# Kernel optimization log

Measured on AMD Instinct MI355X. Metric: run time of the kernel, lower is better.

## Reference

```python
import jax, jax.numpy as jnp
import numpy as np

# ---- constants from init_kwargs (mode='local', channel='G') ----
MEAN = 127.5
STD = 50.0
BINS = np.array([-2.4, -1.6, -0.8, 0.0, 0.8, 1.6, 2.4])
NB = len(BINS) + 1            # 8 quantization levels
DIST = [1, 2, 3]
THETA = [0.0, np.pi / 4, np.pi / 2, 3 * np.pi / 4]
MASK = 17
STRIDE = 4
BIN_EDGES = 0.5 + BINS / 6.0
# skimage greycomatrix offsets: (round(sin(t)*d), round(cos(t)*d)), ordered d-major
OFFSETS = [(int(np.round(np.sin(t) * d)), int(np.round(np.cos(t) * d)))
           for d in DIST for t in THETA]


def setup_inputs() -> dict:
    key = jax.random.key(0)
    x = jax.random.uniform(key, (8, 3, 256, 256), dtype=jnp.float32) * 255.0
    return {"x": x}


def _features(x):
    img = x[:, 1, :, :]                       # channel 'G'
    img = jnp.where(img < 10.0, 0.0, img)     # imgs[imgs < 10] = 0
    B, H, W = img.shape
    N = (H - MASK) // STRIDE + 1              # 60 windows per axis

    # sliding windows -> (B, N, N, MASK, MASK)
    r = (jnp.arange(N) * STRIDE)[:, None] + jnp.arange(MASK)[None, :]
    win = img[:, r[:, None, :, None], r[None, :, None, :]]
    Nw = B * N * N
    flat = win.reshape(Nw, MASK * MASK)

    # ---- stat over nonzero pixels (numpy population std) ----
    mask = flat != 0.0
    n_safe = jnp.maximum(mask.sum(-1), 1).astype(flat.dtype)
    mean = jnp.where(mask, flat, 0.0).sum(-1) / n_safe
    std = jnp.sqrt((jnp.where(mask, flat - mean[:, None], 0.0) ** 2).sum(-1) / n_safe)
    mx = jnp.where(mask, flat, -jnp.inf).max(-1)
    mn = jnp.where(mask, flat, jnp.inf).min(-1)
    stat = jnp.stack([mean, std, (mx - mean) / (std + 1e-9), (mean - mn) / (std + 1e-9)], -1)

    # ---- quantize ----
    q = jnp.digitize(((flat - MEAN) / STD + 3.0) / 6.0, jnp.asarray(BIN_EDGES, flat.dtype))

    # ---- histogram (density over ALL pixels, drop first & last bin) ----
    onehot = (q[..., None] == jnp.arange(NB)).astype(flat.dtype)
    hist_feat = onehot.sum(1)[:, 1:NB - 1] / flat.shape[1]   # (Nw, len(BINS)-1)

    # ---- GLCM per (dist, theta) offset, symmetric + normed ----
    qm = q.reshape(Nw, MASK, MASK)
    rows = jnp.arange(Nw)[:, None]
    glcms = []
    for dr, dc in OFFSETS:
        if dc >= 0:
            i = qm[:, :MASK - dr, :MASK - dc]
            j = qm[:, dr:, dc:]
        else:
            i = qm[:, :MASK - dr, -dc:]
            j = qm[:, dr:, :MASK + dc]
        pair = (i * NB + j).reshape(Nw, -1)
        cnt = jnp.zeros((Nw, NB * NB), flat.dtype).at[rows, pair].add(1.0)
        P = cnt.reshape(Nw, NB, NB)
        P = P + P.transpose(0, 2, 1)                               # symmetric
        P = P / jnp.maximum(P.sum((1, 2), keepdims=True), 1e-12)   # normed
        glcms.append(P)
    G = jnp.stack(glcms, 1)          # (Nw, 12, NB, NB)
    g = G[:, :, 1:, 1:]              # crop level 0 (zeros)
    L = NB - 1

    # greycoprops renormalizes the (cropped) GLCM internally
    Pn = g / jnp.maximum(g.sum((2, 3), keepdims=True), 1e-12)
    I = jnp.arange(L, dtype=flat.dtype)
    diff2 = (I[:, None] - I[None, :]) ** 2
    contrast = (Pn * diff2).sum((2, 3))
    homog = (Pn / (1.0 + diff2)).sum((2, 3))
    energy = jnp.sqrt((Pn ** 2).sum((2, 3)))
    Pi = Pn.sum(3)
    Pj = Pn.sum(2)
    mui = (Pi * I).sum(-1)
    muj = (Pj * I).sum(-1)
    sdi = jnp.sqrt((Pi * (I - mui[..., None]) ** 2).sum(-1))
    sdj = jnp.sqrt((Pj * (I - muj[..., None]) ** 2).sum(-1))
    cov = (Pn * (I[:, None] - mui[..., None, None]) * (I[None, :] - muj[..., None, None])).sum((2, 3))
    corr = jnp.where(sdi * sdj < 1e-15, 1.0, cov / jnp.maximum(sdi * sdj, 1e-15))
    entropy = -(g * jnp.log2(g + 1e-8)).sum((2, 3))   # on cropped, non-renormed g

    glcm_feat = jnp.concatenate([contrast, homog, energy, corr, entropy], -1)  # (Nw, 60)
    feats = jnp.concatenate([stat, hist_feat, glcm_feat], -1)                  # (Nw, 70)

    # windows with max == 0 yield all-zero feature vectors
    feats = jnp.where((flat.max(-1) == 0.0)[:, None], 0.0, feats)

    Fdim = feats.shape[-1]
    feats = feats.reshape(B, N, N, Fdim)
    total = feats.sum((1, 2))
    nz = (feats != 0).sum((1, 2)).astype(flat.dtype)
    return total / (nz + 1e-9)            # (B, 70)


def reference(x):
    return _features(x)
```

## Files before the change

### kernel.cpp

```cpp
#include <hip/hip_runtime.h>
#include <cmath>

#define NPIX   289
#define NU     10
#define NF     70
#define NWX    60
#define IMG_W  256
#define IMG_HW 65536
#define NWIN   28800
#define ACC    560
#define WPB    4
#define NBLK   (NWIN / WPB)

__device__ __constant__ int c_s2u[12] = {0,1,2,3,4,1,5,3,6,7,8,9};

constexpr int DRu[NU] = {0, 1, 1, 1, 0, 2, 0, 2, 3, 2};
constexpr int DCu[NU] = {1, 1, 0,-1, 2, 0, 3, 2, 0,-2};
constexpr int JOFF[NU] = {1, 18, 17, 16, 2, 34, 3, 36, 51, 32};
constexpr float INV2N[NU] = {1.f/544.f, 1.f/512.f, 1.f/544.f, 1.f/512.f, 1.f/510.f,
                             1.f/510.f, 1.f/476.f, 1.f/450.f, 1.f/476.f, 1.f/450.f};

struct CMs { unsigned m[10]; };
constexpr CMs mkcm(int dc) {
    CMs c{};
    for (int t = 0; t < NPIX; ++t) {
        int col = t % 17;
        bool ok = (dc > 0) ? (col >= dc) : (col <= 16 + dc);
        if (ok) c.m[t >> 5] |= 1u << (t & 31);
    }
    return c;
}
constexpr CMs CMp1 = mkcm(1), CMp2 = mkcm(2), CMp3 = mkcm(3);
constexpr CMs CMn1 = mkcm(-1), CMn2 = mkcm(-2);

struct alignas(32) FtE { float w, d2, inv, si, sii, sij, q0, q1; };
struct FtTab { FtE e[28]; };
constexpr FtTab mkft() {
    FtTab t{};
    int n = 0;
    for (int a = 1; a <= 7; ++a)
        for (int b = a; b <= 7; ++b) {
            int i = a - 1, j = b - 1;
            float w  = (a == b) ? 1.f : 2.f;
            float d2 = (float)((i - j) * (i - j));
            t.e[n] = FtE{w, d2, 1.f / (1.f + d2),
                         0.5f * (float)(i + j),
                         0.5f * (float)(i * i + j * j),
                         (float)(i * j), 0.f, 0.f};
            ++n;
        }
    return t;
}
__device__ __constant__ FtTab c_ft = mkft();

template<int O>
__device__ __forceinline__ int gcnt(const unsigned* M, const unsigned* ma) {
    constexpr int wq = JOFF[O] >> 5;
    constexpr int rr = JOFF[O] & 31;
    int acc = 0;
#pragma unroll
    for (int w = 0; w < 9; ++w) {
        unsigned sh = (rr == 0) ? M[w + wq]
                    : __builtin_amdgcn_alignbit(M[w + wq + 1], M[w + wq], rr);
        acc += __popc(ma[w] & sh);
    }
    return acc;
}

__device__ __forceinline__ float wsum(float v){ for(int o=32;o;o>>=1) v += __shfl_xor(v,o,64); return v; }
__device__ __forceinline__ float wmax(float v){ for(int o=32;o;o>>=1) v = fmaxf(v,__shfl_xor(v,o,64)); return v; }
__device__ __forceinline__ float wmin(float v){ for(int o=32;o;o>>=1) v = fminf(v,__shfl_xor(v,o,64)); return v; }

__global__ __launch_bounds__(256, 4) void feat_kernel(const float* __restrict__ x,
                                                      float* __restrict__ ptot,
                                                      float* __restrict__ pnz,
                                                      int setmask) {
    __shared__ float s_g[WPB][NU * 28];
    __shared__ float s_uf[WPB][5][NU];
    __shared__ float s_s10[WPB][10];

    const int lane = threadIdx.x & 63;
    const int wid  = threadIdx.x >> 6;
    const int widx = blockIdx.x * WPB + wid;
    const int b    = widx / 3600;
    const int rem  = widx - b * 3600;
    const int wy   = rem / NWX;
    const int wx   = rem - wy * NWX;
    const float* img = x + (size_t)(b * 3 + 1) * IMG_HW + (wy * 4) * IMG_W + wx * 4;

    float* gl  = s_g[wid];
    float (*uf)[NU] = s_uf[wid];
    float* s10 = s_s10[wid];

    const int l49 = (lane < 49) ? lane : 48;
    const int ba  = l49 / 7 + 1;
    const int bb  = l49 - (ba - 1) * 7 + 1;
    const unsigned long long xm0a = (ba & 1) ? 0ull : ~0ull;
    const unsigned long long xm1a = (ba & 2) ? 0ull : ~0ull;
    const unsigned long long xm2a = (ba & 4) ? 0ull : ~0ull;
    const unsigned long long xm0b = (bb & 1) ? 0ull : ~0ull;
    const unsigned long long xm1b = (bb & 2) ? 0ull : ~0ull;
    const unsigned long long xm2b = (bb & 4) ? 0ull : ~0ull;

    float lsum = 0.f, lss = 0.f, lmax = -1e30f, lmin = 1e30f;
    int n = 0, c1 = 0, c2 = 0, c3 = 0, c4 = 0, c5 = 0, c6 = 0;
    unsigned ma32[10], mb32[12];
#pragma unroll
    for (int k = 0; k < 5; ++k) {
        const int t = lane + k * 64;
        float val = 0.f;
        if (t < NPIX) {
            const int r = t / 17;
            float p = img[r * (IMG_W - 17) + t];
            val = (p < 10.f) ? 0.f : p;
        }
        int qq = min((int)fmaf(val, 0.025f, 0.8125f), 7);
        lsum += val;
        float d = (val != 0.f) ? (val - 127.5f) : 0.f;
        lss = fmaf(d, d, lss);
        lmax = fmaxf(lmax, val);
        lmin = fminf(lmin, (val != 0.f) ? val : 1e30f);
        unsigned long long p0 = __ballot(qq & 1);
        unsigned long long p1 = __ballot(qq & 2);
        unsigned long long p2 = __ballot(qq & 4);
        n  += __popcll(p0 | p1 | p2);
        c1 += __popcll(p0 & ~p1 & ~p2);
        c2 += __popcll(~p0 & p1 & ~p2);
        c3 += __popcll(p0 & p1 & ~p2);
        c4 += __popcll(~p0 & ~p1 & p2);
        c5 += __popcll(p0 & ~p1 & p2);
        c6 += __popcll(~p0 & p1 & p2);
        unsigned long long mA = (p0 ^ xm0a) & (p1 ^ xm1a) & (p2 ^ xm2a);
        unsigned long long mB = (p0 ^ xm0b) & (p1 ^ xm1b) & (p2 ^ xm2b);
        ma32[2*k]   = (unsigned)mA;  ma32[2*k+1] = (unsigned)(mA >> 32);
        mb32[2*k]   = (unsigned)mB;  mb32[2*k+1] = (unsigned)(mB >> 32);
    }
    mb32[10] = 0u; mb32[11] = 0u;

    if (n == 0) return;

    const float fn   = (float)n;
    const float sum  = wsum(lsum);
    const float ss   = wsum(lss);
    const float mx   = wmax(lmax);
    const float mn   = wmin(lmin);
    const float mean = sum / fn;
    const float mc   = mean - 127.5f;
    const float var  = fmaxf(ss / fn - mc * mc, 0.f);
    const float stdv = sqrtf(var);

    if (lane == 0) {
        s10[0] = mean;
        s10[1] = stdv;
        s10[2] = (mx - mean) / (stdv + 1e-9f);
        s10[3] = (mean - mn) / (stdv + 1e-9f);
        s10[4] = (float)c1 * (1.f / 289.f);
        s10[5] = (float)c2 * (1.f / 289.f);
        s10[6] = (float)c3 * (1.f / 289.f);
        s10[7] = (float)c4 * (1.f / 289.f);
        s10[8] = (float)c5 * (1.f / 289.f);
        s10[9] = (float)c6 * (1.f / 289.f);
    }

    int cnta[NU];
    {
        unsigned mv[12]; mv[10] = 0u; mv[11] = 0u;
        cnta[2] = gcnt<2>(mb32, ma32);
        cnta[5] = gcnt<5>(mb32, ma32);
        cnta[8] = gcnt<8>(mb32, ma32);
#pragma unroll
        for (int w = 0; w < 10; ++w) mv[w] = mb32[w] & CMp1.m[w];
        cnta[0] = gcnt<0>(mv, ma32);
        cnta[1] = gcnt<1>(mv, ma32);
#pragma unroll
        for (int w = 0; w < 10; ++w) mv[w] = mb32[w] & CMp2.m[w];
        cnta[4] = gcnt<4>(mv, ma32);
        cnta[7] = gcnt<7>(mv, ma32);
#pragma unroll
        for (int w = 0; w < 10; ++w) mv[w] = mb32[w] & CMp3.m[w];
        cnta[6] = gcnt<6>(mv, ma32);
#pragma unroll
        for (int w = 0; w < 10; ++w) mv[w] = mb32[w] & CMn1.m[w];
        cnta[3] = gcnt<3>(mv, ma32);
#pragma unroll
        for (int w = 0; w < 10; ++w) mv[w] = mb32[w] & CMn2.m[w];
        cnta[9] = gcnt<9>(mv, ma32);
    }

    const int partner = (bb - 1) * 7 + (ba - 1);
    const int amin  = min(ba, bb);
    const int idx28 = 8 * (amin - 1) - ((amin * (amin - 1)) >> 1) + (max(ba, bb) - amin);
    const bool wr   = (lane < 49) && (ba <= bb);
#pragma unroll
    for (int o = 0; o < NU; ++o) {
        int pc = __shfl(cnta[o], partner, 64);
        float g = (float)(cnta[o] + pc) * INV2N[o];
        if (wr) gl[o * 28 + idx28] = g;
    }

    const int fo  = lane & 15;
    const int sub = lane >> 4;
    float gsum=0.f, entU=0.f, conU=0.f, homU=0.f, g2=0.f, siU=0.f, siiU=0.f, sijU=0.f;
    if (fo < NU) {
#pragma unroll
        for (int i = 0; i < 7; ++i) {
            const int e = sub + 4 * i;
            FtE c = c_ft.e[e];
            float g  = gl[fo * 28 + e];
            float gw = g * c.w;
            float l  = __log2f(g + 1e-8f);
            gsum += gw;
            entU  = fmaf(gw, l,      entU);
            conU  = fmaf(gw, c.d2,   conU);
            homU  = fmaf(gw, c.inv,  homU);
            g2    = fmaf(gw, g,      g2);
            siU   = fmaf(gw, c.si,   siU);
            siiU  = fmaf(gw, c.sii,  siiU);
            sijU  = fmaf(gw, c.sij,  sijU);
        }
    }
#pragma unroll
    for (int s = 16; s <= 32; s <<= 1) {
        gsum += __shfl_xor(gsum, s, 64);  entU += __shfl_xor(entU, s, 64);
        conU += __shfl_xor(conU, s, 64);  homU += __shfl_xor(homU, s, 64);
        g2   += __shfl_xor(g2,   s, 64);  siU  += __shfl_xor(siU,  s, 64);
        siiU += __shfl_xor(siiU, s, 64);  sijU += __shfl_xor(sijU, s, 64);
    }
    if (fo < NU && sub == 0) {
        const float invg = 1.f / fmaxf(gsum, 1e-12f);
        const float si  = siU  * invg;
        const float sii = siiU * invg;
        const float sij = sijU * invg;
        const float varg = fmaxf(sii - si * si, 0.f);
        const float cov  = sij - si * si;
        uf[0][fo] = conU * invg;
        uf[1][fo] = homU * invg;
        uf[2][fo] = sqrtf(g2) * invg;
        uf[3][fo] = (varg < 1e-15f) ? 1.f : cov / fmaxf(varg, 1e-15f);
        uf[4][fo] = -entU;
    }

    const int setbase = (widx & setmask) * ACC;
    const int obase   = b * NF;
    for (int t = lane; t < NF; t += 64) {
        float f;
        if (t < 10) {
            f = s10[t];
        } else {
            int u    = t - 10;
            int grp  = u / 12;
            int slot = u - grp * 12;
            f = uf[grp][c_s2u[slot]];
        }
        if (f != 0.f) {
            atomicAdd(&ptot[setbase + obase + t], f);
            atomicAdd(&pnz[setbase + obase + t], 1.f);
        }
    }
}

__global__ void reduce_kernel(const float* __restrict__ ptot,
                              const float* __restrict__ pnz,
                              float* __restrict__ out, int nset) {
    int t = blockIdx.x * blockDim.x + threadIdx.x;
    if (t >= ACC) return;
    float s = 0.f, nz = 0.f;
    for (int k = 0; k < nset; ++k) {
        s  += ptot[(size_t)k * ACC + t];
        nz += pnz[(size_t)k * ACC + t];
    }
    out[t] = s / (nz + 1e-9f);
}

extern "C" void kernel_launch(void* const* d_in, const int* in_sizes, int n_in,
                              void* d_out, int out_size, void* d_ws, size_t ws_size,
                              hipStream_t stream) {
    (void)in_sizes; (void)n_in; (void)out_size;
    const float* x = (const float*)d_in[0];
    float* out = (float*)d_out;

    const size_t per_set = (size_t)2 * ACC * sizeof(float);
    int maxs = (ws_size >= per_set) ? (int)(ws_size / per_set) : 1;
    int nset = 1;
    while ((nset * 2) <= maxs && nset < 64) nset <<= 1;

    float* ptot = (float*)d_ws;
    float* pnz  = ptot + (size_t)nset * ACC;

    hipMemsetAsync(d_ws, 0, (size_t)nset * per_set, stream);
    feat_kernel<<<dim3(NBLK), dim3(256), 0, stream>>>(x, ptot, pnz, nset - 1);
    reduce_kernel<<<dim3((ACC + 255) / 256), dim3(256), 0, stream>>>(ptot, pnz, out, nset);
}
```

Measured before the change: 123.7 us.

## Use DPP wave reductions, bpermute partner masks, trimmed popcount loops, padded LDS

Replaces the shuffle-based wave reductions with DPP row operations followed by a readlane, and uses ds_bpermute for the partner-lane exchanges. Each lane no longer builds the second bin mask from the ballots; it fetches its partner lane's mask through bpermute instead, which saves per-iteration ALU work and registers. The popcount loop is trimmed to the words each offset can actually reach, the quantization clamp is dropped, and the shared GLCM stride is padded to 29 to avoid bank conflicts. The partner-mask swap relies on the symmetric lane mapping, and the DPP reductions depend on the row broadcast semantics being correct on this hardware.

```diff
diff --git a/kernel.cpp b/kernel.cpp
--- a/kernel.cpp
+++ b/kernel.cpp
@@ -11,11 +11,10 @@
 #define ACC    560
 #define WPB    4
 #define NBLK   (NWIN / WPB)
+#define GLS    29
 
 __device__ __constant__ int c_s2u[12] = {0,1,2,3,4,1,5,3,6,7,8,9};
 
-constexpr int DRu[NU] = {0, 1, 1, 1, 0, 2, 0, 2, 3, 2};
-constexpr int DCu[NU] = {1, 1, 0,-1, 2, 0, 3, 2, 0,-2};
 constexpr int JOFF[NU] = {1, 18, 17, 16, 2, 34, 3, 36, 51, 32};
 constexpr float INV2N[NU] = {1.f/544.f, 1.f/512.f, 1.f/544.f, 1.f/512.f, 1.f/510.f,
                              1.f/510.f, 1.f/476.f, 1.f/450.f, 1.f/476.f, 1.f/450.f};
@@ -54,28 +53,61 @@
 __device__ __constant__ FtTab c_ft = mkft();
 
 template<int O>
-__device__ __forceinline__ int gcnt(const unsigned* M, const unsigned* ma) {
+__device__ __forceinline__ int gcnt(const unsigned* __restrict__ M,
+                                    const unsigned* __restrict__ ma) {
     constexpr int wq = JOFF[O] >> 5;
     constexpr int rr = JOFF[O] & 31;
+    constexpr int nw = (288 - JOFF[O]) / 32 + 1;
     int acc = 0;
 #pragma unroll
-    for (int w = 0; w < 9; ++w) {
+    for (int w = 0; w < nw; ++w) {
         unsigned sh = (rr == 0) ? M[w + wq]
-                    : __builtin_amdgcn_alignbit(M[w + wq + 1], M[w + wq], rr);
+                                : __builtin_amdgcn_alignbit(M[w + wq + 1], M[w + wq], rr);
         acc += __popc(ma[w] & sh);
     }
     return acc;
 }
 
-__device__ __forceinline__ float wsum(float v){ for(int o=32;o;o>>=1) v += __shfl_xor(v,o,64); return v; }
-__device__ __forceinline__ float wmax(float v){ for(int o=32;o;o>>=1) v = fmaxf(v,__shfl_xor(v,o,64)); return v; }
-__device__ __forceinline__ float wmin(float v){ for(int o=32;o;o>>=1) v = fminf(v,__shfl_xor(v,o,64)); return v; }
+#define DPP_F(oldv, srcv, ctrl, rm) \
+    __int_as_float(__builtin_amdgcn_update_dpp((oldv), __float_as_int(srcv), (ctrl), (rm), 0xF, false))
+
+__device__ __forceinline__ float dpp_wsum(float v) {
+    v += DPP_F(0, v, 0x111, 0xF);
+    v += DPP_F(0, v, 0x112, 0xF);
+    v += DPP_F(0, v, 0x114, 0xF);
+    v += DPP_F(0, v, 0x118, 0xF);
+    v += DPP_F(0, v, 0x142, 0xA);
+    v += DPP_F(0, v, 0x143, 0xC);
+    return __int_as_float(__builtin_amdgcn_readlane(__float_as_int(v), 63));
+}
+__device__ __forceinline__ float dpp_wmax(float v) {
+    v = fmaxf(v, DPP_F(__float_as_int(v), v, 0x111, 0xF));
+    v = fmaxf(v, DPP_F(__float_as_int(v), v, 0x112, 0xF));
+    v = fmaxf(v, DPP_F(__float_as_int(v), v, 0x114, 0xF));
+    v = fmaxf(v, DPP_F(__float_as_int(v), v, 0x118, 0xF));
+    v = fmaxf(v, DPP_F(__float_as_int(v), v, 0x142, 0xA));
+    v = fmaxf(v, DPP_F(__float_as_int(v), v, 0x143, 0xC));
+    return __int_as_float(__builtin_amdgcn_readlane(__float_as_int(v), 63));
+}
+__device__ __forceinline__ float dpp_wmin(float v) {
+    v = fminf(v, DPP_F(__float_as_int(v), v, 0x111, 0xF));
+    v = fminf(v, DPP_F(__float_as_int(v), v, 0x112, 0xF));
+    v = fminf(v, DPP_F(__float_as_int(v), v, 0x114, 0xF));
+    v = fminf(v, DPP_F(__float_as_int(v), v, 0x118, 0xF));
+    v = fminf(v, DPP_F(__float_as_int(v), v, 0x142, 0xA));
+    v = fminf(v, DPP_F(__float_as_int(v), v, 0x143, 0xC));
+    return __int_as_float(__builtin_amdgcn_readlane(__float_as_int(v), 63));
+}
+
+__device__ __forceinline__ float bperm_f(int addr, float v) {
+    return __int_as_float(__builtin_amdgcn_ds_bpermute(addr, __float_as_int(v)));
+}
 
 __global__ __launch_bounds__(256, 4) void feat_kernel(const float* __restrict__ x,
                                                       float* __restrict__ ptot,
                                                       float* __restrict__ pnz,
                                                       int setmask) {
-    __shared__ float s_g[WPB][NU * 28];
+    __shared__ float s_g[WPB][NU * GLS];
     __shared__ float s_uf[WPB][5][NU];
     __shared__ float s_s10[WPB][10];
 
@@ -95,26 +127,32 @@
     const int l49 = (lane < 49) ? lane : 48;
     const int ba  = l49 / 7 + 1;
     const int bb  = l49 - (ba - 1) * 7 + 1;
+    const int partner = (bb - 1) * 7 + (ba - 1);
+    const int paddr   = partner << 2;
     const unsigned long long xm0a = (ba & 1) ? 0ull : ~0ull;
     const unsigned long long xm1a = (ba & 2) ? 0ull : ~0ull;
     const unsigned long long xm2a = (ba & 4) ? 0ull : ~0ull;
-    const unsigned long long xm0b = (bb & 1) ? 0ull : ~0ull;
-    const unsigned long long xm1b = (bb & 2) ? 0ull : ~0ull;
-    const unsigned long long xm2b = (bb & 4) ? 0ull : ~0ull;
 
     float lsum = 0.f, lss = 0.f, lmax = -1e30f, lmin = 1e30f;
     int n = 0, c1 = 0, c2 = 0, c3 = 0, c4 = 0, c5 = 0, c6 = 0;
-    unsigned ma32[10], mb32[12];
+    unsigned ma32[10];
 #pragma unroll
     for (int k = 0; k < 5; ++k) {
         const int t = lane + k * 64;
-        float val = 0.f;
-        if (t < NPIX) {
+        float val;
+        if (k < 4) {
             const int r = t / 17;
             float p = img[r * (IMG_W - 17) + t];
             val = (p < 10.f) ? 0.f : p;
-        }
-        int qq = min((int)fmaf(val, 0.025f, 0.8125f), 7);
+        } else {
+            float p = 0.f;
+            if (t < NPIX) {
+                const int r = t / 17;
+                p = img[r * (IMG_W - 17) + t];
+            }
+            val = (p < 10.f) ? 0.f : p;
+        }
+        int qq = (int)fmaf(val, 0.025f, 0.8125f);
         lsum += val;
         float d = (val != 0.f) ? (val - 127.5f) : 0.f;
         lss = fmaf(d, d, lss);
@@ -131,19 +169,22 @@
         c5 += __popcll(p0 & ~p1 & p2);
         c6 += __popcll(~p0 & p1 & p2);
         unsigned long long mA = (p0 ^ xm0a) & (p1 ^ xm1a) & (p2 ^ xm2a);
-        unsigned long long mB = (p0 ^ xm0b) & (p1 ^ xm1b) & (p2 ^ xm2b);
-        ma32[2*k]   = (unsigned)mA;  ma32[2*k+1] = (unsigned)(mA >> 32);
-        mb32[2*k]   = (unsigned)mB;  mb32[2*k+1] = (unsigned)(mB >> 32);
-    }
-    mb32[10] = 0u; mb32[11] = 0u;
+        ma32[2*k]   = (unsigned)mA;
+        ma32[2*k+1] = (unsigned)(mA >> 32);
+    }
 
     if (n == 0) return;
 
+    unsigned mv0[10];
+#pragma unroll
+    for (int w = 0; w < 10; ++w)
+        mv0[w] = (unsigned)__builtin_amdgcn_ds_bpermute(paddr, (int)ma32[w]);
+
     const float fn   = (float)n;
-    const float sum  = wsum(lsum);
-    const float ss   = wsum(lss);
-    const float mx   = wmax(lmax);
-    const float mn   = wmin(lmin);
+    const float sum  = dpp_wsum(lsum);
+    const float ss   = dpp_wsum(lss);
+    const float mx   = dpp_wmax(lmax);
+    const float mn   = dpp_wmin(lmin);
     const float mean = sum / fn;
     const float mc   = mean - 127.5f;
     const float var  = fmaxf(ss / fn - mc * mc, 0.f);
@@ -164,38 +205,37 @@
 
     int cnta[NU];
     {
-        unsigned mv[12]; mv[10] = 0u; mv[11] = 0u;
-        cnta[2] = gcnt<2>(mb32, ma32);
-        cnta[5] = gcnt<5>(mb32, ma32);
-        cnta[8] = gcnt<8>(mb32, ma32);
-#pragma unroll
-        for (int w = 0; w < 10; ++w) mv[w] = mb32[w] & CMp1.m[w];
+        cnta[2] = gcnt<2>(mv0, ma32);
+        cnta[5] = gcnt<5>(mv0, ma32);
+        cnta[8] = gcnt<8>(mv0, ma32);
+        unsigned mv[10];
+#pragma unroll
+        for (int w = 0; w < 10; ++w) mv[w] = mv0[w] & CMp1.m[w];
         cnta[0] = gcnt<0>(mv, ma32);
         cnta[1] = gcnt<1>(mv, ma32);
 #pragma unroll
-        for (int w = 0; w < 10; ++w) mv[w] = mb32[w] & CMp2.m[w];
+        for (int w = 0; w < 10; ++w) mv[w] = mv0[w] & CMp2.m[w];
         cnta[4] = gcnt<4>(mv, ma32);
         cnta[7] = gcnt<7>(mv, ma32);
 #pragma unroll
-        for (int w = 0; w < 10; ++w) mv[w] = mb32[w] & CMp3.m[w];
+        for (int w = 0; w < 10; ++w) mv[w] = mv0[w] & CMp3.m[w];
         cnta[6] = gcnt<6>(mv, ma32);
 #pragma unroll
-        for (int w = 0; w < 10; ++w) mv[w] = mb32[w] & CMn1.m[w];
+        for (int w = 0; w < 10; ++w) mv[w] = mv0[w] & CMn1.m[w];
         cnta[3] = gcnt<3>(mv, ma32);
 #pragma unroll
-        for (int w = 0; w < 10; ++w) mv[w] = mb32[w] & CMn2.m[w];
+        for (int w = 0; w < 10; ++w) mv[w] = mv0[w] & CMn2.m[w];
         cnta[9] = gcnt<9>(mv, ma32);
     }
 
-    const int partner = (bb - 1) * 7 + (ba - 1);
     const int amin  = min(ba, bb);
     const int idx28 = 8 * (amin - 1) - ((amin * (amin - 1)) >> 1) + (max(ba, bb) - amin);
     const bool wr   = (lane < 49) && (ba <= bb);
 #pragma unroll
     for (int o = 0; o < NU; ++o) {
-        int pc = __shfl(cnta[o], partner, 64);
+        int pc = __builtin_amdgcn_ds_bpermute(paddr, cnta[o]);
         float g = (float)(cnta[o] + pc) * INV2N[o];
-        if (wr) gl[o * 28 + idx28] = g;
+        if (wr) gl[o * GLS + idx28] = g;
     }
 
     const int fo  = lane & 15;
@@ -206,7 +246,7 @@
         for (int i = 0; i < 7; ++i) {
             const int e = sub + 4 * i;
             FtE c = c_ft.e[e];
-            float g  = gl[fo * 28 + e];
+            float g  = gl[fo * GLS + e];
             float gw = g * c.w;
             float l  = __log2f(g + 1e-8f);
             gsum += gw;
@@ -219,13 +259,17 @@
             sijU  = fmaf(gw, c.sij,  sijU);
         }
     }
-#pragma unroll
-    for (int s = 16; s <= 32; s <<= 1) {
-        gsum += __shfl_xor(gsum, s, 64);  entU += __shfl_xor(entU, s, 64);
-        conU += __shfl_xor(conU, s, 64);  homU += __shfl_xor(homU, s, 64);
-        g2   += __shfl_xor(g2,   s, 64);  siU  += __shfl_xor(siU,  s, 64);
-        siiU += __shfl_xor(siiU, s, 64);  sijU += __shfl_xor(sijU, s, 64);
-    }
+    const int xa16 = (lane ^ 16) << 2;
+    const int xa32 = (lane ^ 32) << 2;
+    gsum += bperm_f(xa16, gsum);  entU += bperm_f(xa16, entU);
+    conU += bperm_f(xa16, conU);  homU += bperm_f(xa16, homU);
+    g2   += bperm_f(xa16, g2);    siU  += bperm_f(xa16, siU);
+    siiU += bperm_f(xa16, siiU);  sijU += bperm_f(xa16, sijU);
+    gsum += bperm_f(xa32, gsum);  entU += bperm_f(xa32, entU);
+    conU += bperm_f(xa32, conU);  homU += bperm_f(xa32, homU);
+    g2   += bperm_f(xa32, g2);    siU  += bperm_f(xa32, siU);
+    siiU += bperm_f(xa32, siiU);  sijU += bperm_f(xa32, sijU);
+
     if (fo < NU && sub == 0) {
         const float invg = 1.f / fmaxf(gsum, 1e-12f);
         const float si  = siU  * invg;
```

After: 120.4 us. 2.7% less time.
